# Performance work log

Hardware: AMD Instinct MI355X
Metric: run time of the kernel (lower is better)

Reference implementation:

```python
import jax, jax.numpy as jnp
import numpy as np

NG, ND, NC, H = 100000, 50000, 50000, 128

def _sage(x_src, x_dst, src, dst, n_dst, W_l, b_l, W_r):
    # PyG SAGEConv: lin_l(mean over incoming neighbors of x_src) + lin_r(x_dst)
    msg = x_src[src]                                             # [E, H] gather
    s = jax.ops.segment_sum(msg, dst, num_segments=n_dst)        # [n_dst, H]
    cnt = jax.ops.segment_sum(jnp.ones(src.shape, x_src.dtype), dst, num_segments=n_dst)
    mean = s / jnp.maximum(cnt, 1.0)[:, None]
    return mean @ W_l + b_l + x_dst @ W_r


def setup_inputs() -> dict:
    key = jax.random.key(0)
    ks = jax.random.split(key, 12)
    sc = 1.0 / np.sqrt(H)
    return {
        'emb_gene': jax.random.normal(ks[0], (NG, H), jnp.float32) * 0.02,
        'emb_disease': jax.random.normal(ks[1], (ND, H), jnp.float32) * 0.02,
        'emb_compound': jax.random.normal(ks[2], (NC, H), jnp.float32) * 0.02,
        'Wl': jax.random.normal(ks[3], (2, 4, H, H), jnp.float32) * sc,
        'bl': jnp.zeros((2, 4, H), jnp.float32),
        'Wr': jax.random.normal(ks[4], (2, 4, H, H), jnp.float32) * sc,
        'eg_src': jax.random.randint(ks[5], (600000,), 0, NG),
        'eg_dst': jax.random.randint(ks[6], (600000,), 0, NG),
        'ecd_src': jax.random.randint(ks[7], (300000,), 0, NC),
        'ecd_dst': jax.random.randint(ks[8], (300000,), 0, ND),
        'ecg_src': jax.random.randint(ks[9], (600000,), 0, NC),
        'ecg_dst': jax.random.randint(ks[10], (600000,), 0, NG),
        'egc_src': jax.random.randint(ks[11], (600000,), 0, NG),
        'egc_dst': jax.random.randint(jax.random.fold_in(key, 99), (600000,), 0, NC),
    }


def reference(emb_gene, emb_disease, emb_compound, Wl, bl, Wr,
              eg_src, eg_dst, ecd_src, ecd_dst, ecg_src, ecg_dst, egc_src, egc_dst):
    xg, xd, xc = emb_gene, emb_disease, emb_compound
    for L in range(2):
        # to_hetero with aggr='sum': sum per-relation SAGEConv outputs per dst type
        og = (_sage(xg, xg, eg_src, eg_dst, NG, Wl[L, 0], bl[L, 0], Wr[L, 0]) +
              _sage(xc, xg, ecg_src, ecg_dst, NG, Wl[L, 2], bl[L, 2], Wr[L, 2]))
        od = _sage(xc, xd, ecd_src, ecd_dst, ND, Wl[L, 1], bl[L, 1], Wr[L, 1])
        oc = _sage(xg, xc, egc_src, egc_dst, NC, Wl[L, 3], bl[L, 3], Wr[L, 3])
        if L < 1:  # relu between layers (dropout inactive in eval)
            og, od, oc = jax.nn.relu(og), jax.nn.relu(od), jax.nn.relu(oc)
        xg, xd, xc = og, od, oc
    # concatenate node-type outputs [NG+ND+NC, H] for a single output array
    return jnp.concatenate([xg, xd, xc], axis=0)
```

## Files before the change

### kernel.cpp

```cpp
#include <hip/hip_runtime.h>


constexpr int HD = 128;
constexpr int NBMAX = 512;
constexpr int BSTRIDE = 32768;

typedef __attribute__((ext_vector_type(8))) short bf16x8;
typedef __attribute__((ext_vector_type(16))) float f32x16;
typedef __attribute__((ext_vector_type(2))) float f32x2;

__device__ __forceinline__ unsigned short f2bf(float x) {
  unsigned u = __builtin_bit_cast(unsigned, x);
  u += 0x7FFF + ((u >> 16) & 1);
  return (unsigned short)(u >> 16);
}
__device__ __forceinline__ float bf2f(unsigned short h) {
  return __builtin_bit_cast(float, (unsigned)h << 16);
}

__device__ __forceinline__ uint2 pack_fp8x8(const float* v) {
  uint2 o;
  unsigned t;
  t = (unsigned)__builtin_amdgcn_cvt_pk_fp8_f32(v[0] * 16.f, v[1] * 16.f, 0, false);
  t = (unsigned)__builtin_amdgcn_cvt_pk_fp8_f32(v[2] * 16.f, v[3] * 16.f, (int)t, true);
  o.x = t;
  t = (unsigned)__builtin_amdgcn_cvt_pk_fp8_f32(v[4] * 16.f, v[5] * 16.f, 0, false);
  t = (unsigned)__builtin_amdgcn_cvt_pk_fp8_f32(v[6] * 16.f, v[7] * 16.f, (int)t, true);
  o.y = t;
  return o;
}

__global__ __launch_bounds__(256) void k_convert(const float* __restrict__ s0,
                                                 const float* __restrict__ s1,
                                                 const float* __restrict__ s2,
                                                 unsigned short* __restrict__ d0,
                                                 unsigned short* __restrict__ d1,
                                                 unsigned short* __restrict__ d2,
                                                 unsigned char* __restrict__ e0,
                                                 unsigned char* __restrict__ e1,
                                                 unsigned char* __restrict__ e2,
                                                 long long n0, long long n1, long long n2) {
  long long i = ((long long)blockIdx.x * 256 + threadIdx.x) * 8;
  const float* s;
  unsigned short* d;
  unsigned char* e;
  if (i < n0) { s = s0 + i; d = d0 + i; e = e0 + i; }
  else if (i < n0 + n1) { s = s1 + (i - n0); d = d1 + (i - n0); e = e1 + (i - n0); }
  else if (i < n0 + n1 + n2) { s = s2 + (i - n0 - n1); d = d2 + (i - n0 - n1); e = e2 + (i - n0 - n1); }
  else return;
  float4 a = *(const float4*)s;
  float4 b = *(const float4*)(s + 4);
  float v[8] = {a.x, a.y, a.z, a.w, b.x, b.y, b.z, b.w};
  uint4 o;
  o.x = (unsigned)f2bf(v[0]) | ((unsigned)f2bf(v[1]) << 16);
  o.y = (unsigned)f2bf(v[2]) | ((unsigned)f2bf(v[3]) << 16);
  o.z = (unsigned)f2bf(v[4]) | ((unsigned)f2bf(v[5]) << 16);
  o.w = (unsigned)f2bf(v[6]) | ((unsigned)f2bf(v[7]) << 16);
  *(uint4*)d = o;
  *(uint2*)e = pack_fp8x8(v);
}

__global__ __launch_bounds__(256) void k_cvt8(const unsigned short* __restrict__ in,
                                              unsigned char* __restrict__ out8, long long n8) {
  long long i = (long long)blockIdx.x * 256 + threadIdx.x;
  if (i >= n8) return;
  uint4 u = *(const uint4*)(in + i * 8);
  float v[8];
  v[0] = bf2f((unsigned short)(u.x & 0xFFFF)); v[1] = bf2f((unsigned short)(u.x >> 16));
  v[2] = bf2f((unsigned short)(u.y & 0xFFFF)); v[3] = bf2f((unsigned short)(u.y >> 16));
  v[4] = bf2f((unsigned short)(u.z & 0xFFFF)); v[5] = bf2f((unsigned short)(u.z >> 16));
  v[6] = bf2f((unsigned short)(u.w & 0xFFFF)); v[7] = bf2f((unsigned short)(u.w >> 16));
  *(uint2*)(out8 + i * 8) = pack_fp8x8(v);
}

struct GArgs {
  const int* esrc[4];
  const int* edst[4];
  int ebase[5];
  int nbase[4];
};

__global__ __launch_bounds__(256) void k_binA(GArgs ga, int Etot, int NB,
                                              int* __restrict__ bucketCur,
                                              unsigned* __restrict__ binned) {
  __shared__ int hist[NBMAX];
  __shared__ int base[NBMAX];
  const int tid = threadIdx.x;
  for (int b = tid; b < NB; b += 256) hist[b] = 0;
  __syncthreads();
  const int e0 = blockIdx.x * 4096;
  for (int i = tid; i < 4096; i += 256) {
    int e = e0 + i;
    if (e < Etot) {
      int r = (e >= ga.ebase[1]) + (e >= ga.ebase[2]) + (e >= ga.ebase[3]);
      int g = ga.nbase[r] + ga.edst[r][e - ga.ebase[r]];
      atomicAdd(&hist[g >> 10], 1);
    }
  }
  __syncthreads();
  for (int b = tid; b < NB; b += 256) {
    int h = hist[b];
    base[b] = h ? atomicAdd(&bucketCur[b], h) : 0;
    hist[b] = 0;
  }
  __syncthreads();
  for (int i = tid; i < 4096; i += 256) {
    int e = e0 + i;
    if (e < Etot) {
      int r = (e >= ga.ebase[1]) + (e >= ga.ebase[2]) + (e >= ga.ebase[3]);
      int el = e - ga.ebase[r];
      int g = ga.nbase[r] + ga.edst[r][el];
      int b = g >> 10;
      int pos = base[b] + atomicAdd(&hist[b], 1);
      binned[(size_t)b * BSTRIDE + pos] =
          ((unsigned)(g & 1023) << 20) | (unsigned)ga.esrc[r][el];
    }
  }
}

__global__ __launch_bounds__(256) void k_binB(const int* __restrict__ bucketCur,
                                              const unsigned* __restrict__ binned,
                                              int* __restrict__ ptr, int* __restrict__ cnt,
                                              int* __restrict__ ss, int Ntot) {
  const int b = blockIdx.x;
  const int tid = threadIdx.x;
  __shared__ int ncnt[1024];
  __shared__ int noff[1024];
  __shared__ int red[256];
  __shared__ int sbase_s;
  __shared__ int wsum[4], wbase[4];

  int part = 0;
  for (int i = tid; i < b; i += 256) part += bucketCur[i];
  red[tid] = part;
  __syncthreads();
  for (int s = 128; s > 0; s >>= 1) {
    if (tid < s) red[tid] += red[tid + s];
    __syncthreads();
  }
  if (tid == 0) sbase_s = red[0];

  for (int j = tid; j < 1024; j += 256) ncnt[j] = 0;
  __syncthreads();

  const int ecount = bucketCur[b];
  const unsigned* bp = binned + (size_t)b * BSTRIDE;
  for (int i = tid; i < ecount; i += 256) atomicAdd(&ncnt[bp[i] >> 20], 1);
  __syncthreads();

  const int j0 = tid * 4;
  int c0 = ncnt[j0], c1 = ncnt[j0 + 1], c2 = ncnt[j0 + 2], c3 = ncnt[j0 + 3];
  int s4 = c0 + c1 + c2 + c3;
  int lane = tid & 63, wid = tid >> 6;
  int incl = s4;
#pragma unroll
  for (int off = 1; off < 64; off <<= 1) {
    int t = __shfl_up(incl, off);
    if (lane >= off) incl += t;
  }
  if (lane == 63) wsum[wid] = incl;
  __syncthreads();
  if (tid == 0) {
    int acc = 0;
#pragma unroll
    for (int w2 = 0; w2 < 4; ++w2) { wbase[w2] = acc; acc += wsum[w2]; }
  }
  __syncthreads();
  int excl = wbase[wid] + incl - s4;
  const int sbase = sbase_s;
  int o0 = excl, o1 = excl + c0, o2 = o1 + c1, o3 = o2 + c2;
  noff[j0] = o0; noff[j0 + 1] = o1; noff[j0 + 2] = o2; noff[j0 + 3] = o3;
  int g0 = b * 1024 + j0;
  if (g0 + 0 < Ntot) { ptr[g0 + 0] = sbase + o0; cnt[g0 + 0] = c0; }
  if (g0 + 1 < Ntot) { ptr[g0 + 1] = sbase + o1; cnt[g0 + 1] = c1; }
  if (g0 + 2 < Ntot) { ptr[g0 + 2] = sbase + o2; cnt[g0 + 2] = c2; }
  if (g0 + 3 < Ntot) { ptr[g0 + 3] = sbase + o3; cnt[g0 + 3] = c3; }
  __syncthreads();

  for (int i = tid; i < ecount; i += 256) {
    unsigned rec = bp[i];
    int j = rec >> 20;
    int p = sbase + atomicAdd(&noff[j], 1);
    ss[p] = (int)(rec & 0xFFFFF);
  }
}

struct AArgs {
  const unsigned char* xs[4];
  unsigned short* mean[4];
  int nbase[4];
  int bbase[5];
  int n[4];
};

__global__ __launch_bounds__(256) void k_aggregate_all(AArgs A, const int* __restrict__ ptr,
                                                       const int* __restrict__ cnt,
                                                       const int* __restrict__ ss) {
  int b = blockIdx.x;
  int r = (b >= A.bbase[1]) + (b >= A.bbase[2]) + (b >= A.bbase[3]);
  int d = (b - A.bbase[r]) * 16 + (threadIdx.x >> 4);
  if (d >= A.n[r]) return;
  const unsigned char* xs = A.xs[r];
  int l = threadIdx.x & 15;
  int g = A.nbase[r] + d;
  int p = ptr[g];
  int deg = cnt[g];
  float a0 = 0.f, a1 = 0.f, a2 = 0.f, a3 = 0.f, a4 = 0.f, a5 = 0.f, a6 = 0.f, a7 = 0.f;
  for (int j0 = 0; j0 < deg; j0 += 16) {
    int m = deg - j0;
    if (m > 16) m = 16;
    int idx = ss[p + j0 + (l < m ? l : m - 1)];
    for (int j = 0; j < m; j += 8) {
      int mm = m - j;
      if (mm > 8) mm = 8;
      uint2 uu[8];
#pragma unroll
      for (int k = 0; k < 8; ++k) {
        if (k < mm) {
          int s = __shfl(idx, j + k, 16);
          uu[k] = *(const uint2*)(xs + (size_t)s * HD + l * 8);
        }
      }
#pragma unroll
      for (int k = 0; k < 8; ++k) {
        if (k < mm) {
          f32x2 p0 = __builtin_amdgcn_cvt_pk_f32_fp8(uu[k].x, false);
          f32x2 p1 = __builtin_amdgcn_cvt_pk_f32_fp8(uu[k].x, true);
          f32x2 p2 = __builtin_amdgcn_cvt_pk_f32_fp8(uu[k].y, false);
          f32x2 p3 = __builtin_amdgcn_cvt_pk_f32_fp8(uu[k].y, true);
          a0 += p0.x; a1 += p0.y; a2 += p1.x; a3 += p1.y;
          a4 += p2.x; a5 += p2.y; a6 += p3.x; a7 += p3.y;
        }
      }
    }
  }
  float inv = 1.0f / (16.0f * (float)(deg > 0 ? deg : 1));
  uint4 o;
  o.x = (unsigned)f2bf(a0 * inv) | ((unsigned)f2bf(a1 * inv) << 16);
  o.y = (unsigned)f2bf(a2 * inv) | ((unsigned)f2bf(a3 * inv) << 16);
  o.z = (unsigned)f2bf(a4 * inv) | ((unsigned)f2bf(a5 * inv) << 16);
  o.w = (unsigned)f2bf(a6 * inv) | ((unsigned)f2bf(a7 * inv) << 16);
  *(uint4*)(A.mean[r] + (size_t)d * HD + l * 8) = o;
}

struct PrepArgs {
  const float* a[14];
  const float* b[14];
};

__global__ __launch_bounds__(256) void k_prepw(PrepArgs pa, unsigned short* __restrict__ out) {
  int s = blockIdx.x;
  const float* A = pa.a[s];
  const float* B = pa.b[s];
  unsigned short* oh = out + (size_t)s * 16384;
  int e0 = blockIdx.y * 1024 + threadIdx.x * 4;
#pragma unroll
  for (int j = 0; j < 4; ++j) {
    int e = e0 + j;
    int k = e >> 7, n = e & 127;
    float v = A[e] + (B ? B[e] : 0.f);
    oh[n * 128 + (k ^ ((n & 15) << 3))] = f2bf(v);
  }
}

struct GemmArgs {
  const unsigned short* x[3][3];
  const unsigned short* wp[3][3];
  const float* b0[3];
  const float* b1[3];
  float* outf[3];
  unsigned short* outb[3];
  int M[3];
  int nslab[3];
  int gbase[4];
  int relu;
};

__global__ __launch_bounds__(256, 2) void k_gemm_all(GemmArgs ga) {
  __shared__ unsigned short ldsb[16384];
  const int t = (blockIdx.x >= ga.gbase[1]) + (blockIdx.x >= ga.gbase[2]);
  const int blk = blockIdx.x - ga.gbase[t];
  const int M = ga.M[t];
  const int nslab = ga.nslab[t];
  const int tid = threadIdx.x;
  const int wave = tid >> 6;
  const int lane = tid & 63;
  const int l31 = lane & 31;
  const int lhalf = lane >> 5;

  const int mbase = blk * 256 + wave * 64;
  int r0 = mbase + l31;
  int r1 = mbase + 32 + l31;
  if (r0 > M - 1) r0 = M - 1;
  if (r1 > M - 1) r1 = M - 1;

  f32x16 acc[2][4];
#pragma unroll
  for (int a = 0; a < 2; ++a)
#pragma unroll
    for (int n = 0; n < 4; ++n)
#pragma unroll
      for (int q = 0; q < 16; ++q) acc[a][n][q] = 0.f;

#pragma unroll
  for (int s = 0; s < 3; ++s) {
    if (s < nslab) {
      const unsigned short* xp = ga.x[t][s];
      __syncthreads();
      {
        const float4* src = (const float4*)ga.wp[t][s];
        float4* dst = (float4*)ldsb;
#pragma unroll
        for (int j = 0; j < 8; ++j) dst[tid + j * 256] = src[tid + j * 256];
      }
      __syncthreads();

#pragma unroll
      for (int ks = 0; ks < 8; ++ks) {
        const int k0 = ks * 16 + lhalf * 8;
        bf16x8 a0 = *(const bf16x8*)(xp + (size_t)r0 * HD + k0);
        bf16x8 a1 = *(const bf16x8*)(xp + (size_t)r1 * HD + k0);
#pragma unroll
        for (int nt = 0; nt < 4; ++nt) {
          const int rown = nt * 32 + l31;
          const int kidx = k0 ^ ((rown & 15) << 3);
          const bf16x8 bb = *(const bf16x8*)&ldsb[rown * HD + kidx];
          acc[0][nt] = __builtin_amdgcn_mfma_f32_32x32x16_bf16(a0, bb, acc[0][nt], 0, 0, 0);
          acc[1][nt] = __builtin_amdgcn_mfma_f32_32x32x16_bf16(a1, bb, acc[1][nt], 0, 0, 0);
        }
      }
    }
  }

  const float* b0 = ga.b0[t];
  const float* b1 = ga.b1[t];
  float* outf = ga.outf[t];
  unsigned short* outb = ga.outb[t];
#pragma unroll
  for (int nt = 0; nt < 4; ++nt) {
    const int col = nt * 32 + l31;
    float bias = b0[col] + (b1 ? b1[col] : 0.f);
#pragma unroll
    for (int as = 0; as < 2; ++as) {
#pragma unroll
      for (int rg = 0; rg < 16; ++rg) {
        int row = mbase + as * 32 + (rg & 3) + 8 * (rg >> 2) + 4 * lhalf;
        float v = acc[as][nt][rg] + bias;
        if (ga.relu) v = fmaxf(v, 0.f);
        if (row < M) {
          if (outf) outf[(size_t)row * HD + col] = v;
          else outb[(size_t)row * HD + col] = f2bf(v);
        }
      }
    }
  }
}

extern "C" void kernel_launch(void* const* d_in, const int* in_sizes, int n_in,
                              void* d_out, int out_size, void* d_ws, size_t ws_size,
                              hipStream_t stream) {
  const float* emb_g = (const float*)d_in[0];
  const float* emb_d = (const float*)d_in[1];
  const float* emb_c = (const float*)d_in[2];
  const float* Wl = (const float*)d_in[3];
  const float* bl = (const float*)d_in[4];
  const float* Wr = (const float*)d_in[5];

  const int NG = in_sizes[0] / HD;
  const int ND = in_sizes[1] / HD;
  const int NC = in_sizes[2] / HD;
  const int E0 = in_sizes[6];
  const int E1 = in_sizes[8];
  const int E2 = in_sizes[10];
  const int E3 = in_sizes[12];
  const int HH = HD * HD;
  const int Etot = E0 + E1 + E2 + E3;
  const int Ntot = NG + ND + NG + NC;
  const int NB = (Ntot + 1023) >> 10;

  char* w = (char*)d_ws;
  unsigned short* wprep = (unsigned short*)w; w += (size_t)14 * 32768;
  unsigned short* xbf_g0 = (unsigned short*)w; w += (size_t)NG * HD * 2;
  unsigned short* xbf_d0 = (unsigned short*)w; w += (size_t)ND * HD * 2;
  unsigned short* xbf_c0 = (unsigned short*)w; w += (size_t)NC * HD * 2;
  unsigned short* xbf_g1 = (unsigned short*)w; w += (size_t)NG * HD * 2;
  unsigned short* xbf_d1 = (unsigned short*)w; w += (size_t)ND * HD * 2;
  unsigned short* xbf_c1 = (unsigned short*)w; w += (size_t)NC * HD * 2;
  unsigned short* mean_gg = (unsigned short*)w; w += (size_t)NG * HD * 2;
  unsigned short* mean_cd = (unsigned short*)w; w += (size_t)ND * HD * 2;
  unsigned short* mean_cg = (unsigned short*)w; w += (size_t)NG * HD * 2;
  unsigned short* mean_gc = (unsigned short*)w; w += (size_t)NC * HD * 2;
  unsigned char* x8_g0 = (unsigned char*)w; w += (size_t)NG * HD;
  unsigned char* x8_d0 = (unsigned char*)w; w += (size_t)ND * HD;
  unsigned char* x8_c0 = (unsigned char*)w; w += (size_t)NC * HD;
  unsigned char* x8_g1 = (unsigned char*)w; w += (size_t)NG * HD;
  unsigned char* x8_d1 = (unsigned char*)w; w += (size_t)ND * HD;
  unsigned char* x8_c1 = (unsigned char*)w; w += (size_t)NC * HD;
  int* ss = (int*)w;        w += (size_t)Etot * 4;
  int* ptr = (int*)w;       w += (size_t)Ntot * 4;
  int* cnt = (int*)w;       w += (size_t)Ntot * 4;
  unsigned* binned = (unsigned*)w; w += (size_t)NB * BSTRIDE * 4;
  int* bucketCur = (int*)w; w += (size_t)NBMAX * 4;

  hipMemsetAsync(bucketCur, 0, (size_t)NBMAX * 4, stream);

  {
    long long n0 = (long long)NG * HD, n1 = (long long)ND * HD, n2 = (long long)NC * HD;
    long long tot8 = (n0 + n1 + n2) / 8;
    k_convert<<<(int)((tot8 + 255) / 256), 256, 0, stream>>>(
        emb_g, emb_d, emb_c, xbf_g0, xbf_d0, xbf_c0, x8_g0, x8_d0, x8_c0, n0, n1, n2);
  }

  GArgs ga;
  ga.esrc[0] = (const int*)d_in[6];  ga.edst[0] = (const int*)d_in[7];
  ga.esrc[1] = (const int*)d_in[8];  ga.edst[1] = (const int*)d_in[9];
  ga.esrc[2] = (const int*)d_in[10]; ga.edst[2] = (const int*)d_in[11];
  ga.esrc[3] = (const int*)d_in[12]; ga.edst[3] = (const int*)d_in[13];
  ga.ebase[0] = 0; ga.ebase[1] = E0; ga.ebase[2] = E0 + E1;
  ga.ebase[3] = E0 + E1 + E2; ga.ebase[4] = Etot;
  ga.nbase[0] = 0; ga.nbase[1] = NG; ga.nbase[2] = NG + ND; ga.nbase[3] = NG + ND + NG;

  k_binA<<<(Etot + 4095) / 4096, 256, 0, stream>>>(ga, Etot, NB, bucketCur, binned);
  k_binB<<<NB, 256, 0, stream>>>(bucketCur, binned, ptr, cnt, ss, Ntot);

  PrepArgs pa;
  for (int L = 0; L < 2; ++L) {
    int b = L * 7;
    pa.a[b + 0] = Wl + (size_t)(L * 4 + 0) * HH; pa.b[b + 0] = nullptr;
    pa.a[b + 1] = Wl + (size_t)(L * 4 + 2) * HH; pa.b[b + 1] = nullptr;
    pa.a[b + 2] = Wr + (size_t)(L * 4 + 0) * HH; pa.b[b + 2] = Wr + (size_t)(L * 4 + 2) * HH;
    pa.a[b + 3] = Wl + (size_t)(L * 4 + 1) * HH; pa.b[b + 3] = nullptr;
    pa.a[b + 4] = Wr + (size_t)(L * 4 + 1) * HH; pa.b[b + 4] = nullptr;
    pa.a[b + 5] = Wl + (size_t)(L * 4 + 3) * HH; pa.b[b + 5] = nullptr;
    pa.a[b + 6] = Wr + (size_t)(L * 4 + 3) * HH; pa.b[b + 6] = nullptr;
  }
  k_prepw<<<dim3(14, 16), 256, 0, stream>>>(pa, wprep);

  float* out = (float*)d_out;
  float* xg_out = out;
  float* xd_out = out + (size_t)NG * HD;
  float* xc_out = out + (size_t)(NG + ND) * HD;

  for (int L = 0; L < 2; ++L) {
    const unsigned short* xg = L ? xbf_g1 : xbf_g0;
    const unsigned short* xd = L ? xbf_d1 : xbf_d0;
    const unsigned short* xc = L ? xbf_c1 : xbf_c0;
    const unsigned char* x8g = L ? x8_g1 : x8_g0;
    const unsigned char* x8c = L ? x8_c1 : x8_c0;

    if (L == 1) {
      long long n8 = ((long long)(NG + ND + NC) * HD) / 8;
      k_cvt8<<<(int)((n8 + 255) / 256), 256, 0, stream>>>(xbf_g1, x8_g1, n8);
    }

    AArgs aa;
    aa.xs[0] = x8g; aa.xs[1] = x8c; aa.xs[2] = x8c; aa.xs[3] = x8g;
    aa.mean[0] = mean_gg; aa.mean[1] = mean_cd; aa.mean[2] = mean_cg; aa.mean[3] = mean_gc;
    aa.nbase[0] = 0; aa.nbase[1] = NG; aa.nbase[2] = NG + ND; aa.nbase[3] = NG + ND + NG;
    aa.n[0] = NG; aa.n[1] = ND; aa.n[2] = NG; aa.n[3] = NC;
    int bb = 0;
    for (int r = 0; r < 4; ++r) { aa.bbase[r] = bb; bb += (aa.n[r] + 15) / 16; }
    aa.bbase[4] = bb;
    k_aggregate_all<<<bb, 256, 0, stream>>>(aa, ptr, cnt, ss);

    const float* bl_L = bl + (size_t)L * 4 * HD;
    const unsigned short* wp = wprep + (size_t)L * 7 * 16384;

    GemmArgs gm;
    gm.x[0][0] = mean_gg; gm.x[0][1] = mean_cg; gm.x[0][2] = xg;
    gm.wp[0][0] = wp + 0 * 16384; gm.wp[0][1] = wp + 1 * 16384; gm.wp[0][2] = wp + 2 * 16384;
    gm.b0[0] = bl_L + 0 * HD; gm.b1[0] = bl_L + 2 * HD;
    gm.M[0] = NG; gm.nslab[0] = 3;
    gm.x[1][0] = mean_cd; gm.x[1][1] = xd; gm.x[1][2] = nullptr;
    gm.wp[1][0] = wp + 3 * 16384; gm.wp[1][1] = wp + 4 * 16384; gm.wp[1][2] = nullptr;
    gm.b0[1] = bl_L + 1 * HD; gm.b1[1] = nullptr;
    gm.M[1] = ND; gm.nslab[1] = 2;
    gm.x[2][0] = mean_gc; gm.x[2][1] = xc; gm.x[2][2] = nullptr;
    gm.wp[2][0] = wp + 5 * 16384; gm.wp[2][1] = wp + 6 * 16384; gm.wp[2][2] = nullptr;
    gm.b0[2] = bl_L + 3 * HD; gm.b1[2] = nullptr;
    gm.M[2] = NC; gm.nslab[2] = 2;
    if (L) {
      gm.outf[0] = xg_out; gm.outf[1] = xd_out; gm.outf[2] = xc_out;
      gm.outb[0] = gm.outb[1] = gm.outb[2] = nullptr;
    } else {
      gm.outf[0] = gm.outf[1] = gm.outf[2] = nullptr;
      gm.outb[0] = xbf_g1; gm.outb[1] = xbf_d1; gm.outb[2] = xbf_c1;
    }
    gm.relu = (L == 0) ? 1 : 0;
    int gb = 0;
    for (int t = 0; t < 3; ++t) { gm.gbase[t] = gb; gb += (gm.M[t] + 255) / 256; }
    gm.gbase[3] = gb;
    k_gemm_all<<<gb, 256, 0, stream>>>(gm);
  }
}
```

Baseline: 382.9 us.

## Fuse fp8 activation conversion into GEMM epilogue and shrink GEMM row tile

Drops the standalone bf16-to-fp8 conversion kernel between layers and instead writes fp8 copies of gene and compound activations in the layer-0 GEMM epilogue, skipping the unused disease fp8 buffer. The GEMM is retiled to 128 rows per block with one 32-row MFMA strip per wave, and launch bounds now allow more blocks per CU. This removes a full read/write pass over the activations and a launch, but it adds byte-granular scattered stores in the epilogue and reloads the weight slab into LDS twice as often.

After: 374.0 us. -2.3%, faster.

```diff
diff --git a/kernel.cpp b/kernel.cpp
--- a/kernel.cpp
+++ b/kernel.cpp
@@ -60,19 +60,6 @@
   *(uint2*)e = pack_fp8x8(v);
 }
 
-__global__ __launch_bounds__(256) void k_cvt8(const unsigned short* __restrict__ in,
-                                              unsigned char* __restrict__ out8, long long n8) {
-  long long i = (long long)blockIdx.x * 256 + threadIdx.x;
-  if (i >= n8) return;
-  uint4 u = *(const uint4*)(in + i * 8);
-  float v[8];
-  v[0] = bf2f((unsigned short)(u.x & 0xFFFF)); v[1] = bf2f((unsigned short)(u.x >> 16));
-  v[2] = bf2f((unsigned short)(u.y & 0xFFFF)); v[3] = bf2f((unsigned short)(u.y >> 16));
-  v[4] = bf2f((unsigned short)(u.z & 0xFFFF)); v[5] = bf2f((unsigned short)(u.z >> 16));
-  v[6] = bf2f((unsigned short)(u.w & 0xFFFF)); v[7] = bf2f((unsigned short)(u.w >> 16));
-  *(uint2*)(out8 + i * 8) = pack_fp8x8(v);
-}
-
 struct GArgs {
   const int* esrc[4];
   const int* edst[4];
@@ -270,13 +257,14 @@
   const float* b1[3];
   float* outf[3];
   unsigned short* outb[3];
+  unsigned char* out8[3];
   int M[3];
   int nslab[3];
   int gbase[4];
   int relu;
 };
 
-__global__ __launch_bounds__(256, 2) void k_gemm_all(GemmArgs ga) {
+__global__ __launch_bounds__(256, 4) void k_gemm_all(GemmArgs ga) {
   __shared__ unsigned short ldsb[16384];
   const int t = (blockIdx.x >= ga.gbase[1]) + (blockIdx.x >= ga.gbase[2]);
   const int blk = blockIdx.x - ga.gbase[t];
@@ -288,19 +276,15 @@
   const int l31 = lane & 31;
   const int lhalf = lane >> 5;
 
-  const int mbase = blk * 256 + wave * 64;
+  const int mbase = blk * 128 + wave * 32;
   int r0 = mbase + l31;
-  int r1 = mbase + 32 + l31;
   if (r0 > M - 1) r0 = M - 1;
-  if (r1 > M - 1) r1 = M - 1;
-
-  f32x16 acc[2][4];
-#pragma unroll
-  for (int a = 0; a < 2; ++a)
-#pragma unroll
-    for (int n = 0; n < 4; ++n)
-#pragma unroll
-      for (int q = 0; q < 16; ++q) acc[a][n][q] = 0.f;
+
+  f32x16 acc[4];
+#pragma unroll
+  for (int n = 0; n < 4; ++n)
+#pragma unroll
+    for (int q = 0; q < 16; ++q) acc[n][q] = 0.f;
 
 #pragma unroll
   for (int s = 0; s < 3; ++s) {
@@ -319,14 +303,12 @@
       for (int ks = 0; ks < 8; ++ks) {
         const int k0 = ks * 16 + lhalf * 8;
         bf16x8 a0 = *(const bf16x8*)(xp + (size_t)r0 * HD + k0);
-        bf16x8 a1 = *(const bf16x8*)(xp + (size_t)r1 * HD + k0);
 #pragma unroll
         for (int nt = 0; nt < 4; ++nt) {
           const int rown = nt * 32 + l31;
           const int kidx = k0 ^ ((rown & 15) << 3);
           const bf16x8 bb = *(const bf16x8*)&ldsb[rown * HD + kidx];
-          acc[0][nt] = __builtin_amdgcn_mfma_f32_32x32x16_bf16(a0, bb, acc[0][nt], 0, 0, 0);
-          acc[1][nt] = __builtin_amdgcn_mfma_f32_32x32x16_bf16(a1, bb, acc[1][nt], 0, 0, 0);
+          acc[nt] = __builtin_amdgcn_mfma_f32_32x32x16_bf16(a0, bb, acc[nt], 0, 0, 0);
         }
       }
     }
@@ -336,20 +318,27 @@
   const float* b1 = ga.b1[t];
   float* outf = ga.outf[t];
   unsigned short* outb = ga.outb[t];
+  unsigned char* out8 = ga.out8[t];
 #pragma unroll
   for (int nt = 0; nt < 4; ++nt) {
     const int col = nt * 32 + l31;
     float bias = b0[col] + (b1 ? b1[col] : 0.f);
 #pragma unroll
-    for (int as = 0; as < 2; ++as) {
-#pragma unroll
-      for (int rg = 0; rg < 16; ++rg) {
-        int row = mbase + as * 32 + (rg & 3) + 8 * (rg >> 2) + 4 * lhalf;
-        float v = acc[as][nt][rg] + bias;
-        if (ga.relu) v = fmaxf(v, 0.f);
-        if (row < M) {
-          if (outf) outf[(size_t)row * HD + col] = v;
-          else outb[(size_t)row * HD + col] = f2bf(v);
+    for (int rg = 0; rg < 16; ++rg) {
+      int row = mbase + (rg & 3) + 8 * (rg >> 2) + 4 * lhalf;
+      float v = acc[nt][rg] + bias;
+      if (ga.relu) v = fmaxf(v, 0.f);
+      if (row < M) {
+        if (outf) {
+          outf[(size_t)row * HD + col] = v;
+        } else {
+          unsigned short h = f2bf(v);
+          outb[(size_t)row * HD + col] = h;
+          if (out8) {
+            float vb = bf2f(h);
+            unsigned pk = (unsigned)__builtin_amdgcn_cvt_pk_fp8_f32(vb * 16.f, vb * 16.f, 0, false);
+            out8[(size_t)row * HD + col] = (unsigned char)(pk & 0xFF);
+          }
         }
       }
     }
@@ -394,7 +383,6 @@
   unsigned char* x8_d0 = (unsigned char*)w; w += (size_t)ND * HD;
   unsigned char* x8_c0 = (unsigned char*)w; w += (size_t)NC * HD;
   unsigned char* x8_g1 = (unsigned char*)w; w += (size_t)NG * HD;
-  unsigned char* x8_d1 = (unsigned char*)w; w += (size_t)ND * HD;
   unsigned char* x8_c1 = (unsigned char*)w; w += (size_t)NC * HD;
   int* ss = (int*)w;        w += (size_t)Etot * 4;
   int* ptr = (int*)w;       w += (size_t)Ntot * 4;
@@ -447,11 +435,6 @@
     const unsigned short* xc = L ? xbf_c1 : xbf_c0;
     const unsigned char* x8g = L ? x8_g1 : x8_g0;
     const unsigned char* x8c = L ? x8_c1 : x8_c0;
-
-    if (L == 1) {
-      long long n8 = ((long long)(NG + ND + NC) * HD) / 8;
-      k_cvt8<<<(int)((n8 + 255) / 256), 256, 0, stream>>>(xbf_g1, x8_g1, n8);
-    }
 
     AArgs aa;
     aa.xs[0] = x8g; aa.xs[1] = x8c; aa.xs[2] = x8c; aa.xs[3] = x8g;
@@ -482,13 +465,15 @@
     if (L) {
       gm.outf[0] = xg_out; gm.outf[1] = xd_out; gm.outf[2] = xc_out;
       gm.outb[0] = gm.outb[1] = gm.outb[2] = nullptr;
+      gm.out8[0] = gm.out8[1] = gm.out8[2] = nullptr;
     } else {
       gm.outf[0] = gm.outf[1] = gm.outf[2] = nullptr;
       gm.outb[0] = xbf_g1; gm.outb[1] = xbf_d1; gm.outb[2] = xbf_c1;
+      gm.out8[0] = x8_g1; gm.out8[1] = nullptr; gm.out8[2] = x8_c1;
     }
     gm.relu = (L == 0) ? 1 : 0;
     int gb = 0;
-    for (int t = 0; t < 3; ++t) { gm.gbase[t] = gb; gb += (gm.M[t] + 255) / 256; }
+    for (int t = 0; t < 3; ++t) { gm.gbase[t] = gb; gb += (gm.M[t] + 127) / 128; }
     gm.gbase[3] = gb;
     k_gemm_all<<<gb, 256, 0, stream>>>(gm);
   }
```
